# Optimization experiments

Hardware: AMD Instinct MI355X
Metric: run time of the kernel (lower is better)

## Reference

```python
import jax, jax.numpy as jnp
import numpy as np

P = 2        # patch size (all 3 dims)
NB = 8       # num_bands
N = 16       # d_state
DTR = 8      # dt_rank = d_model // 16
DCONV = 4    # d_conv
SMAX = 2.0   # smax_dt = smax_B = smax_C


def _ln(x, g, b):
    mu = x.mean(-1, keepdims=True)
    v = ((x - mu) ** 2).mean(-1, keepdims=True)
    return (x - mu) / jnp.sqrt(v + 1e-5) * g + b


def _silu(x):
    return x * jax.nn.sigmoid(x)


def _ssm_layer(x, band, m, rho, Win, bin_, convw, convb, Wx, Wdt, bdt, Alog, Dp,
               Wout, bout, edt, eB, eC, wr, wm):
    # x: [B, L, d_model] -> bidirectional conditioned selective scan (BiFCSSM)
    Bsz, L, _ = x.shape
    ED = convw.shape[0]
    xz = x @ Win + bin_
    xp, z = xz[..., :ED], xz[..., ED:]
    # depthwise causal conv1d over L
    xpad = jnp.pad(xp, ((0, 0), (DCONV - 1, 0), (0, 0)))
    xc = sum(xpad[:, k:k + L, :] * convw[:, k] for k in range(DCONV)) + convb
    xc = _silu(xc)
    dbl = xc @ Wx                                    # [B,L,DTR+2N]
    dt = jax.nn.softplus(dbl[..., :DTR] @ Wdt + bdt)  # [B,L,ED]
    # band/radius/mask conditioned modulation of delta, B, C
    s_dt = SMAX * jax.nn.sigmoid(edt[band][None] + wr[0] * rho[None] + wm[0] * m)
    s_B = SMAX * jax.nn.sigmoid(eB[band][None] + wr[1] * rho[None] + wm[1] * m)
    s_C = SMAX * jax.nn.sigmoid(eC[band][None] + wr[2] * rho[None] + wm[2] * m)
    dt = dt * s_dt[..., None]
    Bm = dbl[..., DTR:DTR + N] * s_B[..., None]       # [B,L,N]
    Cm = dbl[..., DTR + N:] * s_C[..., None]          # [B,L,N]
    A = -jnp.exp(Alog)                                # [ED,N]
    dA = jnp.exp(dt[..., None] * A)                   # [B,L,ED,N]
    dBu = (dA - 1.0) / A * Bm[:, :, None, :] * xc[..., None]   # exact ZOH
    dA_s = jnp.moveaxis(dA, 1, 0)
    dBu_s = jnp.moveaxis(dBu, 1, 0)
    C_s = jnp.moveaxis(Cm, 1, 0)
    h0 = jnp.zeros((Bsz, ED, N), x.dtype)

    def step(h, inp):
        a, bu, c = inp
        h = a * h + bu
        return h, jnp.einsum('ben,bn->be', h, c)

    _, yf = jax.lax.scan(step, h0, (dA_s, dBu_s, C_s))
    _, yb = jax.lax.scan(step, h0, (dA_s, dBu_s, C_s), reverse=True)
    y = jnp.moveaxis(yf + yb, 0, 1) + Dp * xc
    y = y * _silu(z)
    return y @ Wout + bout


def _fwd(kspace_ri, mask, pe_w, pe_b, pu_w, pu_b, ln_g, ln_b, fn_g, fn_b,
         cond_band, cond_rad_w, cond_mask_w, l0_Win, l0_bin, l0_convw, l0_convb,
         l0_Wx, l0_Wdt, l0_bdt, l0_Alog, l0_D, l0_Wout, l0_bout, l0_edt, l0_eB,
         l0_eC, l0_wr, l0_wm):
    Bsz, C, nx, ny, nz = kspace_ri.shape
    gx, gy, gz = nx // P, ny // P, nz // P
    L = gx * gy * gz
    # patch embed (Conv3d, kernel==stride) as blocked einsum
    xr = kspace_ri.reshape(Bsz, C, gx, P, gy, P, gz, P)
    x = jnp.einsum('bcxiyjzk,dcijk->bdxyz', xr, pe_w) + pe_b[None, :, None, None, None]
    DM = x.shape[1]
    x = x.reshape(Bsz, DM, L).transpose(0, 2, 1)               # [B,L,D]
    m = mask.reshape(Bsz, 1, gx, P, gy, P, gz, P).mean(axis=(3, 5, 7)).reshape(Bsz, L)
    m = jnp.clip(m, 0.0, 1.0)
    # raster scan ordering: identity permutation, rho_bar, band ids
    rho = jnp.arange(L, dtype=x.dtype) / float(L - 1)
    band = jnp.clip(jnp.floor(rho * NB).astype(jnp.int32), 0, NB - 1)
    # condition tokens
    cond = cond_band[band][None] + rho[None, :, None] * cond_rad_w + m[:, :, None] * cond_mask_w
    h = _ln(x + cond, ln_g, ln_b)
    h = h + _ssm_layer(_ln(h, fn_g, fn_b), band, m, rho, l0_Win, l0_bin, l0_convw,
                       l0_convb, l0_Wx, l0_Wdt, l0_bdt, l0_Alog, l0_D, l0_Wout,
                       l0_bout, l0_edt, l0_eB, l0_eC, l0_wr, l0_wm)
    # patch unembed (ConvTranspose3d, kernel==stride) as blocked einsum
    hg = h.transpose(0, 2, 1).reshape(Bsz, DM, gx, gy, gz)
    out = jnp.einsum('bdxyz,dcijk->bcxiyjzk', hg, pu_w).reshape(Bsz, C, nx, ny, nz)
    out = out + pu_b[None, :, None, None, None]
    return kspace_ri + out


def setup_inputs() -> dict:
    key = jax.random.key(0)
    ks = jax.random.split(key, 24)
    ED, DM, CIN = 256, 128, 16

    def nrm(k, shape, s):
        return jax.random.normal(k, shape, jnp.float32) * s

    return {
        'kspace_ri': jax.random.normal(ks[0], (1, CIN, 64, 64, 16), jnp.float32),
        'mask': jax.random.uniform(ks[1], (1, 1, 64, 64, 16), jnp.float32),
        'pe_w': nrm(ks[2], (DM, CIN, P, P, P), 0.09),
        'pe_b': nrm(ks[3], (DM,), 0.02),
        'pu_w': nrm(ks[4], (DM, CIN, P, P, P), 0.05),
        'pu_b': jnp.zeros((CIN,), jnp.float32),
        'ln_g': jnp.ones((DM,), jnp.float32),
        'ln_b': jnp.zeros((DM,), jnp.float32),
        'fn_g': jnp.ones((DM,), jnp.float32),
        'fn_b': jnp.zeros((DM,), jnp.float32),
        'cond_band': nrm(ks[5], (NB, DM), 0.02),
        'cond_rad_w': nrm(ks[6], (DM,), 0.02),
        'cond_mask_w': nrm(ks[7], (DM,), 0.02),
        'l0_Win': nrm(ks[8], (DM, 2 * ED), 0.05),
        'l0_bin': jnp.zeros((2 * ED,), jnp.float32),
        'l0_convw': nrm(ks[9], (ED, DCONV), 0.2),
        'l0_convb': jnp.zeros((ED,), jnp.float32),
        'l0_Wx': nrm(ks[10], (ED, DTR + 2 * N), 0.05),
        'l0_Wdt': nrm(ks[11], (DTR, ED), 0.1),
        'l0_bdt': jnp.full((ED,), -3.0, jnp.float32),
        'l0_Alog': jnp.log(jnp.tile(jnp.arange(1, N + 1, dtype=jnp.float32), (ED, 1))),
        'l0_D': jnp.ones((ED,), jnp.float32),
        'l0_Wout': nrm(ks[12], (ED, DM), 0.05),
        'l0_bout': jnp.zeros((DM,), jnp.float32),
        'l0_edt': nrm(ks[13], (NB,), 0.1),
        'l0_eB': nrm(ks[14], (NB,), 0.1),
        'l0_eC': nrm(ks[15], (NB,), 0.1),
        'l0_wr': nrm(ks[16], (3,), 0.1),
        'l0_wm': nrm(ks[17], (3,), 0.1),
    }


def reference(kspace_ri, mask, pe_w, pe_b, pu_w, pu_b, ln_g, ln_b, fn_g, fn_b,
              cond_band, cond_rad_w, cond_mask_w, l0_Win, l0_bin, l0_convw,
              l0_convb, l0_Wx, l0_Wdt, l0_bdt, l0_Alog, l0_D, l0_Wout, l0_bout,
              l0_edt, l0_eB, l0_eC, l0_wr, l0_wm):
    return _fwd(kspace_ri, mask, pe_w, pe_b, pu_w, pu_b, ln_g, ln_b, fn_g, fn_b,
                cond_band, cond_rad_w, cond_mask_w, l0_Win, l0_bin, l0_convw,
                l0_convb, l0_Wx, l0_Wdt, l0_bdt, l0_Alog, l0_D, l0_Wout, l0_bout,
                l0_edt, l0_eB, l0_eC, l0_wr, l0_wm)
```

## Files before the change

### kernel.cpp

```cpp
#include <hip/hip_runtime.h>
#include <hip/hip_bf16.h>

#define L_TOK 8192
#define NCh 256
#define CLh 32
#define LOG2E 1.44269504088896f

typedef short bf16x8 __attribute__((ext_vector_type(8)));
typedef float f32x4 __attribute__((ext_vector_type(4)));

static __device__ __forceinline__ float nexp2(float x) {
#if __has_builtin(__builtin_amdgcn_exp2f)
    return __builtin_amdgcn_exp2f(x);
#else
    return exp2f(x);
#endif
}
static __device__ __forceinline__ float sigm(float x) {
    return 1.f / (1.f + nexp2(-x * LOG2E));
}
static __device__ __forceinline__ ushort f2bf(float x) {
    union { float f; uint u; } v; v.f = x;
    uint r = v.u + 0x7fffu + ((v.u >> 16) & 1u);
    return (ushort)(r >> 16);
}
static __device__ __forceinline__ float bf2f(ushort h) {
    union { float f; uint u; } v; v.u = ((uint)h) << 16;
    return v.f;
}
static __device__ __forceinline__ void f2hl(float x, ushort* hi, ushort* lo) {
    ushort h = f2bf(x);
    *hi = h;
    *lo = f2bf(x - bf2f(h));
}

#define W_PE   0
#define W_WIN  16384
#define W_WOUT 81920
#define W_PU   114688
#define W_PROJ 131072
#define W_TOT  212992

__global__ __launch_bounds__(256) void prep_k(const float* __restrict__ pe_w, const float* __restrict__ Win,
                                              const float* __restrict__ Wx, const float* __restrict__ Wdt,
                                              const float* __restrict__ Wout, const float* __restrict__ pu_w,
                                              const float* __restrict__ mask,
                                              ushort* __restrict__ wH, ushort* __restrict__ wL,
                                              float* __restrict__ mbuf) {
    int b = blockIdx.x;
    if (b >= 832) {
        int l = (b - 832) * 256 + threadIdx.x;
        int xg = l >> 8, yg = (l >> 3) & 31, zg = l & 7;
        float s = 0.f;
        for (int i2 = 0; i2 < 2; ++i2)
            for (int j2 = 0; j2 < 2; ++j2)
                for (int k2 = 0; k2 < 2; ++k2)
                    s += mask[(2 * xg + i2) * 1024 + (2 * yg + j2) * 16 + 2 * zg + k2];
        s *= 0.125f;
        mbuf[l] = fminf(fmaxf(s, 0.f), 1.f);
        return;
    }
    int i = b * 256 + threadIdx.x;
    float v;
    if (i < 16384) {
        v = pe_w[i];
    } else if (i < 81920) {
        int j = i - 16384; int n = j >> 7, k = j & 127;
        v = Win[k * 512 + n];
    } else if (i < 114688) {
        int j = i - 81920; int n = j >> 8, k = j & 255;
        v = Wout[k * 128 + n];
    } else if (i < 131072) {
        int j = i - 114688; int n = j >> 7, k = j & 127;
        v = pu_w[k * 128 + n];
    } else {
        int j = i - 131072; int n = j >> 8, k = j & 255;
        if (n < 256) {
            float s = 0.f;
#pragma unroll
            for (int r = 0; r < 8; ++r) s += Wx[k * 40 + r] * Wdt[r * 256 + n];
            v = s;
        } else if (n < 288) {
            v = Wx[k * 40 + 8 + (n - 256)];
        } else {
            v = 0.f;
        }
    }
    ushort h, lo; f2hl(v, &h, &lo);
    wH[i] = h; wL[i] = lo;
}

__global__ __launch_bounds__(256) void embed_ln_k(const float* __restrict__ ks,
                                                  const ushort* __restrict__ wH, const ushort* __restrict__ wL,
                                                  const float* __restrict__ pe_b, const float* __restrict__ cond_band,
                                                  const float* __restrict__ cond_rad, const float* __restrict__ cond_mask,
                                                  const float* __restrict__ mbuf,
                                                  const float* __restrict__ ln_g, const float* __restrict__ ln_b,
                                                  const float* __restrict__ fn_g, const float* __restrict__ fn_b,
                                                  float* __restrict__ h_,
                                                  ushort* __restrict__ hnH, ushort* __restrict__ hnL) {
    __shared__ __align__(16) char smem[50176];
    ushort (*AsH)[72] = (ushort(*)[72])(smem);
    ushort (*AsL)[72] = (ushort(*)[72])(smem + 2304);
    ushort (*BsH)[72] = (ushort(*)[72])(smem + 4608);
    ushort (*BsL)[72] = (ushort(*)[72])(smem + 23040);
    float*  ksb       = (float*)(smem + 41472);
    float  (*Cs)[132] = (float(*)[132])(smem);

    const int tid = threadIdx.x;
    const int lane = tid & 63, wn = tid >> 6;
    const int ln = lane & 15, q = lane >> 4;
    const int mb = blockIdx.x * 16;
    const int xg = mb >> 8, yg0 = (mb >> 3) & 31;

    for (int v = tid; v < 512; v += 256) {
        int seg = v >> 2, zq = v & 3;
        int cc = seg >> 3, i2 = (seg >> 2) & 1, yy = seg & 3;
        float4 t4 = *(const float4*)&ks[cc * 65536 + (2 * xg + i2) * 1024 + (2 * yg0 + yy) * 16 + zq * 4];
        int la = seg * 17 + zq * 4;
        ksb[la] = t4.x; ksb[la + 1] = t4.y; ksb[la + 2] = t4.z; ksb[la + 3] = t4.w;
    }

    f32x4 acc[2];
    acc[0] = (f32x4){0.f, 0.f, 0.f, 0.f};
    acc[1] = (f32x4){0.f, 0.f, 0.f, 0.f};

    for (int kc = 0; kc < 128; kc += 64) {
        __syncthreads();
        for (int u = tid; u < 1024; u += 256) {
            int r = u >> 6, kk = u & 63;
            int k = kc + kk;
            int cc = k >> 3, ijk = k & 7;
            int i2 = (ijk >> 2) & 1, j2 = (ijk >> 1) & 1, k2 = ijk & 1;
            int seg = (cc * 2 + i2) * 4 + (r >> 3) * 2 + j2;
            float v = ksb[seg * 17 + (r & 7) * 2 + k2];
            ushort hh, ll; f2hl(v, &hh, &ll);
            AsH[r][kk] = hh; AsL[r][kk] = ll;
        }
        for (int u = tid; u < 1024; u += 256) {
            int n = u >> 3, g = u & 7;
            *(uint4*)&BsH[n][g * 8] = *(const uint4*)&wH[W_PE + n * 128 + kc + g * 8];
            *(uint4*)&BsL[n][g * 8] = *(const uint4*)&wL[W_PE + n * 128 + kc + g * 8];
        }
        __syncthreads();
#pragma unroll
        for (int ks_ = 0; ks_ < 64; ks_ += 32) {
            const int kk = ks_ + q * 8;
            bf16x8 ah = *(const bf16x8*)&AsH[ln][kk];
            bf16x8 al = *(const bf16x8*)&AsL[ln][kk];
#pragma unroll
            for (int cb = 0; cb < 2; ++cb) {
                bf16x8 bh = *(const bf16x8*)&BsH[wn * 32 + cb * 16 + ln][kk];
                bf16x8 bl = *(const bf16x8*)&BsL[wn * 32 + cb * 16 + ln][kk];
                acc[cb] = __builtin_amdgcn_mfma_f32_16x16x32_bf16(ah, bh, acc[cb], 0, 0, 0);
                acc[cb] = __builtin_amdgcn_mfma_f32_16x16x32_bf16(ah, bl, acc[cb], 0, 0, 0);
                acc[cb] = __builtin_amdgcn_mfma_f32_16x16x32_bf16(al, bh, acc[cb], 0, 0, 0);
            }
        }
    }
    __syncthreads();
#pragma unroll
    for (int cb = 0; cb < 2; ++cb) {
#pragma unroll
        for (int r = 0; r < 4; ++r) {
            int row = q * 4 + r;
            int col = wn * 32 + cb * 16 + ln;
            int l = mb + row;
            float rho = (float)l * (1.0f / 8191.0f);
            int band = min(7, (int)(rho * 8.0f));
            Cs[row][col] = acc[cb][r] + pe_b[col] + cond_band[band * 128 + col]
                           + rho * cond_rad[col] + mbuf[l] * cond_mask[col];
        }
    }
    __syncthreads();
    {
        int row = tid >> 4, j = tid & 15;
        int l = mb + row;
        float v8[8];
        float s = 0.f, s2 = 0.f;
#pragma unroll
        for (int i = 0; i < 8; ++i) {
            float v = Cs[row][j * 8 + i];
            v8[i] = v; s += v; s2 += v * v;
        }
#pragma unroll
        for (int o = 1; o < 16; o <<= 1) { s += __shfl_xor(s, o, 16); s2 += __shfl_xor(s2, o, 16); }
        float mu = s * (1.f / 128.f);
        float var = s2 * (1.f / 128.f) - mu * mu;
        float rstd = rsqrtf(fmaxf(var, 0.f) + 1e-5f);
        float hv[8];
        s = 0.f; s2 = 0.f;
#pragma unroll
        for (int i = 0; i < 8; ++i) {
            int col = j * 8 + i;
            float h = (v8[i] - mu) * rstd * ln_g[col] + ln_b[col];
            hv[i] = h; s += h; s2 += h * h;
        }
#pragma unroll
        for (int i = 0; i < 8; i += 4)
            *(float4*)&h_[(size_t)l * 128 + j * 8 + i] = make_float4(hv[i], hv[i + 1], hv[i + 2], hv[i + 3]);
#pragma unroll
        for (int o = 1; o < 16; o <<= 1) { s += __shfl_xor(s, o, 16); s2 += __shfl_xor(s2, o, 16); }
        mu = s * (1.f / 128.f);
        var = s2 * (1.f / 128.f) - mu * mu;
        rstd = rsqrtf(fmaxf(var, 0.f) + 1e-5f);
        union { ushort u[8]; uint4 v4; } oh, ol;
#pragma unroll
        for (int i = 0; i < 8; ++i) {
            int col = j * 8 + i;
            float o2 = (hv[i] - mu) * rstd * fn_g[col] + fn_b[col];
            ushort hh, ll; f2hl(o2, &hh, &ll);
            oh.u[i] = hh; ol.u[i] = ll;
        }
        *(uint4*)&hnH[(size_t)l * 128 + j * 8] = oh.v4;
        *(uint4*)&hnL[(size_t)l * 128 + j * 8] = ol.v4;
    }
}

__global__ __launch_bounds__(256) void win_k(const ushort* __restrict__ Ah, const ushort* __restrict__ Al,
                                             const ushort* __restrict__ wH, const ushort* __restrict__ wL,
                                             const float* __restrict__ bin_,
                                             float* __restrict__ xp, float* __restrict__ sz) {
    __shared__ ushort AsH[64][72], AsL[64][72];
    __shared__ ushort BsH[64][72], BsL[64][72];
    const int tid = threadIdx.x;
    const int lane = tid & 63, wave = tid >> 6;
    const int wm = wave & 1, wn = wave >> 1;
    const int ln = lane & 15, q = lane >> 4;
    const int mb = blockIdx.x * 64, nb = blockIdx.y * 64;

    f32x4 acc[2][2];
#pragma unroll
    for (int rb = 0; rb < 2; ++rb)
#pragma unroll
        for (int cb = 0; cb < 2; ++cb) acc[rb][cb] = (f32x4){0.f, 0.f, 0.f, 0.f};

    for (int kc = 0; kc < 128; kc += 64) {
        __syncthreads();
        for (int u = tid; u < 512; u += 256) {
            int r = u >> 3, g = u & 7;
            size_t go = (size_t)(mb + r) * 128 + kc + g * 8;
            *(uint4*)&AsH[r][g * 8] = *(const uint4*)&Ah[go];
            *(uint4*)&AsL[r][g * 8] = *(const uint4*)&Al[go];
        }
        for (int u = tid; u < 512; u += 256) {
            int n = u >> 3, g = u & 7;
            size_t go = (size_t)(W_WIN) + (size_t)(nb + n) * 128 + kc + g * 8;
            *(uint4*)&BsH[n][g * 8] = *(const uint4*)&wH[go];
            *(uint4*)&BsL[n][g * 8] = *(const uint4*)&wL[go];
        }
        __syncthreads();
#pragma unroll
        for (int ks_ = 0; ks_ < 64; ks_ += 32) {
            const int kk = ks_ + q * 8;
            bf16x8 ah[2], al[2], bh[2], bl[2];
#pragma unroll
            for (int rb = 0; rb < 2; ++rb) {
                ah[rb] = *(const bf16x8*)&AsH[wm * 32 + rb * 16 + ln][kk];
                al[rb] = *(const bf16x8*)&AsL[wm * 32 + rb * 16 + ln][kk];
            }
#pragma unroll
            for (int cb = 0; cb < 2; ++cb) {
                bh[cb] = *(const bf16x8*)&BsH[wn * 32 + cb * 16 + ln][kk];
                bl[cb] = *(const bf16x8*)&BsL[wn * 32 + cb * 16 + ln][kk];
            }
#pragma unroll
            for (int rb = 0; rb < 2; ++rb)
#pragma unroll
                for (int cb = 0; cb < 2; ++cb) {
                    acc[rb][cb] = __builtin_amdgcn_mfma_f32_16x16x32_bf16(ah[rb], bh[cb], acc[rb][cb], 0, 0, 0);
                    acc[rb][cb] = __builtin_amdgcn_mfma_f32_16x16x32_bf16(ah[rb], bl[cb], acc[rb][cb], 0, 0, 0);
                    acc[rb][cb] = __builtin_amdgcn_mfma_f32_16x16x32_bf16(al[rb], bh[cb], acc[rb][cb], 0, 0, 0);
                }
        }
    }
#pragma unroll
    for (int rb = 0; rb < 2; ++rb)
#pragma unroll
        for (int cb = 0; cb < 2; ++cb)
#pragma unroll
            for (int r = 0; r < 4; ++r) {
                int l = mb + wm * 32 + rb * 16 + q * 4 + r;
                int col = nb + wn * 32 + cb * 16 + ln;
                float v = acc[rb][cb][r] + bin_[col];
                if (col < 256) {
                    xp[(size_t)l * 256 + col] = v;
                } else {
                    sz[(size_t)l * 256 + (col - 256)] = v * sigm(v);
                }
            }
}

__global__ __launch_bounds__(512) void proj_k(const float* __restrict__ xp,
                                              const float* __restrict__ convw, const float* __restrict__ convb,
                                              const ushort* __restrict__ wH, const ushort* __restrict__ wL,
                                              const float* __restrict__ bdt, const float* __restrict__ mbuf,
                                              const float* __restrict__ edt, const float* __restrict__ eB,
                                              const float* __restrict__ eC, const float* __restrict__ wr,
                                              const float* __restrict__ wm,
                                              float* __restrict__ xc, float* __restrict__ dt,
                                              float* __restrict__ Bm, float* __restrict__ Cm) {
    __shared__ __align__(16) char smem[52224];
    ushort (*AsH)[264] = (ushort(*)[264])(smem);
    ushort (*AsL)[264] = (ushort(*)[264])(smem + 16896);
    ushort (*BsH)[72]  = (ushort(*)[72])(smem + 33792);
    ushort (*BsL)[72]  = (ushort(*)[72])(smem + 43008);
    const int tid = threadIdx.x;
    const int mb = blockIdx.x * 32;

    {
        const int cg = tid & 63;
        const int rg = tid >> 6;
        const int c0 = cg * 4;
        float4 cb4 = *(const float4*)&convb[c0];
        float4 cw0 = *(const float4*)&convw[(c0 + 0) * 4];
        float4 cw1 = *(const float4*)&convw[(c0 + 1) * 4];
        float4 cw2 = *(const float4*)&convw[(c0 + 2) * 4];
        float4 cw3 = *(const float4*)&convw[(c0 + 3) * 4];
        const int lbase = mb + rg * 4;
        float4 zero = make_float4(0.f, 0.f, 0.f, 0.f);
        float4 x0 = (lbase - 3 >= 0) ? *(const float4*)&xp[(size_t)(lbase - 3) * 256 + c0] : zero;
        float4 x1 = (lbase - 2 >= 0) ? *(const float4*)&xp[(size_t)(lbase - 2) * 256 + c0] : zero;
        float4 x2 = (lbase - 1 >= 0) ? *(const float4*)&xp[(size_t)(lbase - 1) * 256 + c0] : zero;
#pragma unroll
        for (int rr = 0; rr < 4; ++rr) {
            int l = lbase + rr;
            float4 x3 = *(const float4*)&xp[(size_t)l * 256 + c0];
            float o0 = cb4.x + x0.x * cw0.x + x1.x * cw0.y + x2.x * cw0.z + x3.x * cw0.w;
            float o1 = cb4.y + x0.y * cw1.x + x1.y * cw1.y + x2.y * cw1.z + x3.y * cw1.w;
            float o2 = cb4.z + x0.z * cw2.x + x1.z * cw2.y + x2.z * cw2.z + x3.z * cw2.w;
            float o3 = cb4.w + x0.w * cw3.x + x1.w * cw3.y + x2.w * cw3.z + x3.w * cw3.w;
            o0 *= sigm(o0); o1 *= sigm(o1); o2 *= sigm(o2); o3 *= sigm(o3);
            *(float4*)&xc[(size_t)l * 256 + c0] = make_float4(o0, o1, o2, o3);
            union { ushort u[4]; uint2 v2; } hh, ll;
            f2hl(o0, &hh.u[0], &ll.u[0]); f2hl(o1, &hh.u[1], &ll.u[1]);
            f2hl(o2, &hh.u[2], &ll.u[2]); f2hl(o3, &hh.u[3], &ll.u[3]);
            int row = l - mb;
            *(uint2*)&AsH[row][c0] = hh.v2;
            *(uint2*)&AsL[row][c0] = ll.v2;
            x0 = x1; x1 = x2; x2 = x3;
        }
    }
    __syncthreads();

    const int lane = tid & 63, wave = tid >> 6;
    const int wm2 = wave & 1, wn4 = wave >> 1;
    const int ln = lane & 15, q = lane >> 4;
    for (int it = 0; it < 5; ++it) {
        int nb = it * 64;
        f32x4 acc = (f32x4){0.f, 0.f, 0.f, 0.f};
        for (int kc = 0; kc < 256; kc += 64) {
            __syncthreads();
            {
                int u = tid;
                int n = u >> 3, g = u & 7;
                size_t go = (size_t)(W_PROJ) + (size_t)(nb + n) * 256 + kc + g * 8;
                *(uint4*)&BsH[n][g * 8] = *(const uint4*)&wH[go];
                *(uint4*)&BsL[n][g * 8] = *(const uint4*)&wL[go];
            }
            __syncthreads();
#pragma unroll
            for (int ks_ = 0; ks_ < 64; ks_ += 32) {
                const int kka = kc + ks_ + q * 8;
                const int kkb = ks_ + q * 8;
                bf16x8 ah = *(const bf16x8*)&AsH[wm2 * 16 + ln][kka];
                bf16x8 al = *(const bf16x8*)&AsL[wm2 * 16 + ln][kka];
                bf16x8 bh = *(const bf16x8*)&BsH[wn4 * 16 + ln][kkb];
                bf16x8 bl = *(const bf16x8*)&BsL[wn4 * 16 + ln][kkb];
                acc = __builtin_amdgcn_mfma_f32_16x16x32_bf16(ah, bh, acc, 0, 0, 0);
                acc = __builtin_amdgcn_mfma_f32_16x16x32_bf16(ah, bl, acc, 0, 0, 0);
                acc = __builtin_amdgcn_mfma_f32_16x16x32_bf16(al, bh, acc, 0, 0, 0);
            }
        }
#pragma unroll
        for (int r = 0; r < 4; ++r) {
            int l = mb + wm2 * 16 + q * 4 + r;
            int col = nb + wn4 * 16 + ln;
            float v = acc[r];
            float rho = (float)l * (1.0f / 8191.0f);
            int band = min(7, (int)(rho * 8.0f));
            float mv = mbuf[l];
            if (col < 256) {
                float sc0 = 2.0f * sigm(edt[band] + wr[0] * rho + wm[0] * mv);
                float v2 = v + bdt[col];
                float sp = (v2 > 20.f) ? v2 : log1pf(expf(v2));
                dt[(size_t)l * 256 + col] = sp * sc0;
            } else if (col < 272) {
                float sc1 = 2.0f * sigm(eB[band] + wr[1] * rho + wm[1] * mv);
                Bm[(size_t)l * 16 + (col - 256)] = v * sc1;
            } else if (col < 288) {
                float sc2 = 2.0f * sigm(eC[band] + wr[2] * rho + wm[2] * mv);
                Cm[(size_t)l * 16 + (col - 272)] = v * sc2;
            }
        }
    }
}

__global__ __launch_bounds__(256) void scan0_k(const float* __restrict__ dt, const float* __restrict__ xc,
                                               const float* __restrict__ Bm, const float* __restrict__ Alog,
                                               float* __restrict__ Hb, float* __restrict__ sdtb) {
    const int c = blockIdx.x, dir = blockIdx.y, e = threadIdx.x;
    __shared__ float bms[CLh][16];
    for (int idx = e; idx < CLh * 16; idx += 256)
        bms[idx >> 4][idx & 15] = Bm[c * (CLh * 16) + idx];
    float A2[16], iv[16], h[16];
#pragma unroll
    for (int n = 0; n < 16; ++n) {
        float ea = nexp2(Alog[e * 16 + n] * LOG2E);
        A2[n] = -ea * LOG2E;
        iv[n] = -1.0f / ea;
        h[n] = 0.f;
    }
    const int base = c * CLh;
    float cu[8], cx[8], nu[8], nx[8];
#pragma unroll
    for (int j = 0; j < 8; ++j) {
        int p = dir ? (CLh - 1 - j) : j;
        cu[j] = dt[(size_t)(base + p) * 256 + e];
        cx[j] = xc[(size_t)(base + p) * 256 + e];
    }
    __syncthreads();
    float sdt = 0.f;
#pragma unroll
    for (int g = 0; g < CLh / 8; ++g) {
        if (g + 1 < CLh / 8) {
#pragma unroll
            for (int j = 0; j < 8; ++j) {
                int s = (g + 1) * 8 + j;
                int p = dir ? (CLh - 1 - s) : s;
                nu[j] = dt[(size_t)(base + p) * 256 + e];
                nx[j] = xc[(size_t)(base + p) * 256 + e];
            }
        }
#pragma unroll
        for (int j = 0; j < 8; ++j) {
            int s = g * 8 + j;
            int p = dir ? (CLh - 1 - s) : s;
            float u = cu[j], xv = cx[j];
            union { float4 v[4]; float f[16]; } bb;
            const float4* bp = (const float4*)&bms[p][0];
            bb.v[0] = bp[0]; bb.v[1] = bp[1]; bb.v[2] = bp[2]; bb.v[3] = bp[3];
#pragma unroll
            for (int n = 0; n < 16; ++n) {
                float a = nexp2(A2[n] * u);
                float w = xv * bb.f[n] * iv[n];
                h[n] = a * (h[n] + w) - w;
            }
            sdt += u;
        }
#pragma unroll
        for (int j = 0; j < 8; ++j) { cu[j] = nu[j]; cx[j] = nx[j]; }
    }
    const size_t hofs = (size_t)(dir * NCh + c) * 4096 + e * 16;
#pragma unroll
    for (int j = 0; j < 4; ++j)
        *(float4*)&Hb[hofs + 4 * j] = make_float4(h[4 * j], h[4 * j + 1], h[4 * j + 2], h[4 * j + 3]);
    if (dir == 0) sdtb[c * 256 + e] = sdt;
}

__global__ __launch_bounds__(64) void combine_k(const float* __restrict__ Hb, float* __restrict__ Hpre,
                                                const float* __restrict__ sdtb, const float* __restrict__ Alog) {
    int id = blockIdx.x * 64 + threadIdx.x;
    int dir = id >> 12, en = id & 4095, e = en >> 4;
    float A2 = -nexp2(Alog[en] * LOG2E) * LOG2E;
    float hi = 0.f;
    for (int g = 0; g < NCh / 8; ++g) {
        float Pv[8], qv[8];
#pragma unroll
        for (int j = 0; j < 8; ++j) {
            int c = dir ? (NCh - 1 - (g * 8 + j)) : (g * 8 + j);
            Pv[j] = sdtb[c * 256 + e];
            qv[j] = Hb[(size_t)(dir * NCh + c) * 4096 + en];
        }
#pragma unroll
        for (int j = 0; j < 8; ++j) {
            int c = dir ? (NCh - 1 - (g * 8 + j)) : (g * 8 + j);
            float P = nexp2(A2 * Pv[j]);
            Hpre[(size_t)(dir * NCh + c) * 4096 + en] = hi;
            hi = P * hi + qv[j];
        }
    }
}

template <int DIR>
static __device__ __forceinline__ void scan_dir(const float* __restrict__ dt, const float* __restrict__ xc,
                                                int base, int e,
                                                const float (*bms)[16], const float (*cms)[16],
                                                const float* A2, const float* iv,
                                                float* h, float* yreg) {
    float cu[8], cx[8], nu[8], nx[8];
#pragma unroll
    for (int j = 0; j < 8; ++j) {
        const int p = DIR ? (CLh - 1 - j) : j;
        cu[j] = dt[(size_t)(base + p) * 256 + e];
        cx[j] = xc[(size_t)(base + p) * 256 + e];
    }
#pragma unroll
    for (int g = 0; g < CLh / 8; ++g) {
        if (g + 1 < CLh / 8) {
#pragma unroll
            for (int j = 0; j < 8; ++j) {
                const int s = (g + 1) * 8 + j;
                const int p = DIR ? (CLh - 1 - s) : s;
                nu[j] = dt[(size_t)(base + p) * 256 + e];
                nx[j] = xc[(size_t)(base + p) * 256 + e];
            }
        }
#pragma unroll
        for (int j = 0; j < 8; ++j) {
            const int s = g * 8 + j;
            const int p = DIR ? (CLh - 1 - s) : s;
            float u = cu[j], xv = cx[j];
            union { float4 v[4]; float f[16]; } bb, cc;
            const float4* bp = (const float4*)&bms[p][0];
            bb.v[0] = bp[0]; bb.v[1] = bp[1]; bb.v[2] = bp[2]; bb.v[3] = bp[3];
            const float4* cp = (const float4*)&cms[p][0];
            cc.v[0] = cp[0]; cc.v[1] = cp[1]; cc.v[2] = cp[2]; cc.v[3] = cp[3];
            float y = 0.f;
#pragma unroll
            for (int n = 0; n < 16; ++n) {
                float a = nexp2(A2[n] * u);
                float w = xv * bb.f[n] * iv[n];
                h[n] = a * (h[n] + w) - w;
                y += h[n] * cc.f[n];
            }
            yreg[p] = y;
        }
#pragma unroll
        for (int j = 0; j < 8; ++j) { cu[j] = nu[j]; cx[j] = nx[j]; }
    }
}

__global__ __launch_bounds__(512) void scan1g_k(const float* __restrict__ dt, const float* __restrict__ xc,
                                                const float* __restrict__ Bm, const float* __restrict__ Cm,
                                                const float* __restrict__ Alog, const float* __restrict__ Hpre,
                                                const float* __restrict__ sz, const float* __restrict__ Dp,
                                                ushort* __restrict__ AHo, ushort* __restrict__ ALo) {
    const int c = blockIdx.x;
    const int tid = threadIdx.x;
    const int dir = tid >> 8;
    const int e = tid & 255;
    __shared__ float bms[CLh][16];
    __shared__ float cms[CLh][16];
    __shared__ float ysum[CLh][256];
    for (int idx = tid; idx < CLh * 16; idx += 512) {
        bms[idx >> 4][idx & 15] = Bm[c * (CLh * 16) + idx];
        cms[idx >> 4][idx & 15] = Cm[c * (CLh * 16) + idx];
    }
    float A2[16], iv[16], h[16];
#pragma unroll
    for (int n = 0; n < 16; ++n) {
        float ea = nexp2(Alog[e * 16 + n] * LOG2E);
        A2[n] = -ea * LOG2E;
        iv[n] = -1.0f / ea;
    }
    const size_t hofs = (size_t)(dir * NCh + c) * 4096 + e * 16;
#pragma unroll
    for (int j = 0; j < 4; ++j) {
        float4 hv = *(const float4*)&Hpre[hofs + 4 * j];
        h[4 * j] = hv.x; h[4 * j + 1] = hv.y; h[4 * j + 2] = hv.z; h[4 * j + 3] = hv.w;
    }
    const int base = c * CLh;
    float yreg[CLh];
    __syncthreads();
    if (dir == 0) {
        scan_dir<0>(dt, xc, base, e, bms, cms, A2, iv, h, yreg);
    } else {
        scan_dir<1>(dt, xc, base, e, bms, cms, A2, iv, h, yreg);
    }
    __syncthreads();
    if (dir == 0) {
#pragma unroll
        for (int l = 0; l < CLh; ++l) ysum[l][e] = yreg[l];
    }
    __syncthreads();
    if (dir == 1) {
        float dpv = Dp[e];
#pragma unroll
        for (int l = 0; l < CLh; ++l) {
            size_t gl = (size_t)(base + l) * 256 + e;
            float a = (ysum[l][e] + yreg[l] + dpv * xc[gl]) * sz[gl];
            ushort hh, ll; f2hl(a, &hh, &ll);
            AHo[gl] = hh; ALo[gl] = ll;
        }
    }
}

__global__ __launch_bounds__(256) void wout_k(const ushort* __restrict__ AH, const ushort* __restrict__ AL,
                                              const ushort* __restrict__ wH, const ushort* __restrict__ wL,
                                              const float* __restrict__ bout, const float* __restrict__ h_,
                                              ushort* __restrict__ hfH, ushort* __restrict__ hfL) {
    __shared__ ushort AsH[32][72], AsL[32][72];
    __shared__ ushort BsH[64][72], BsL[64][72];
    const int tid = threadIdx.x;
    const int lane = tid & 63, wave = tid >> 6;
    const int wm = wave & 1, wn = wave >> 1;
    const int ln = lane & 15, q = lane >> 4;
    const int mb = blockIdx.x * 32, nb = blockIdx.y * 64;

    f32x4 acc[2];
    acc[0] = (f32x4){0.f, 0.f, 0.f, 0.f};
    acc[1] = (f32x4){0.f, 0.f, 0.f, 0.f};

    for (int kc = 0; kc < 256; kc += 64) {
        __syncthreads();
        for (int u = tid; u < 256; u += 256) {
            int r = u >> 3, g = u & 7;
            size_t go = (size_t)(mb + r) * 256 + kc + g * 8;
            *(uint4*)&AsH[r][g * 8] = *(const uint4*)&AH[go];
            *(uint4*)&AsL[r][g * 8] = *(const uint4*)&AL[go];
        }
        for (int u = tid; u < 512; u += 256) {
            int n = u >> 3, g = u & 7;
            size_t go = (size_t)(W_WOUT) + (size_t)(nb + n) * 256 + kc + g * 8;
            *(uint4*)&BsH[n][g * 8] = *(const uint4*)&wH[go];
            *(uint4*)&BsL[n][g * 8] = *(const uint4*)&wL[go];
        }
        __syncthreads();
#pragma unroll
        for (int ks_ = 0; ks_ < 64; ks_ += 32) {
            const int kk = ks_ + q * 8;
            bf16x8 ah = *(const bf16x8*)&AsH[wm * 16 + ln][kk];
            bf16x8 al = *(const bf16x8*)&AsL[wm * 16 + ln][kk];
#pragma unroll
            for (int cb = 0; cb < 2; ++cb) {
                bf16x8 bh = *(const bf16x8*)&BsH[wn * 32 + cb * 16 + ln][kk];
                bf16x8 bl = *(const bf16x8*)&BsL[wn * 32 + cb * 16 + ln][kk];
                acc[cb] = __builtin_amdgcn_mfma_f32_16x16x32_bf16(ah, bh, acc[cb], 0, 0, 0);
                acc[cb] = __builtin_amdgcn_mfma_f32_16x16x32_bf16(ah, bl, acc[cb], 0, 0, 0);
                acc[cb] = __builtin_amdgcn_mfma_f32_16x16x32_bf16(al, bh, acc[cb], 0, 0, 0);
            }
        }
    }
#pragma unroll
    for (int cb = 0; cb < 2; ++cb)
#pragma unroll
        for (int r = 0; r < 4; ++r) {
            int l = mb + wm * 16 + q * 4 + r;
            int col = nb + wn * 32 + cb * 16 + ln;
            float v = acc[cb][r] + bout[col] + h_[(size_t)l * 128 + col];
            ushort hh, ll; f2hl(v, &hh, &ll);
            hfH[(size_t)l * 128 + col] = hh;
            hfL[(size_t)l * 128 + col] = ll;
        }
}

__global__ __launch_bounds__(256) void unembed_k(const ushort* __restrict__ Ah, const ushort* __restrict__ Al,
                                                 const ushort* __restrict__ wH, const ushort* __restrict__ wL,
                                                 const float* __restrict__ pu_b, const float* __restrict__ ks,
                                                 float* __restrict__ out) {
    __shared__ ushort AsH[32][72], AsL[32][72];
    __shared__ ushort BsH[64][72], BsL[64][72];
    const int tid = threadIdx.x;
    const int lane = tid & 63, wave = tid >> 6;
    const int wm = wave & 1, wn = wave >> 1;
    const int ln = lane & 15, q = lane >> 4;
    const int mb = blockIdx.x * 32, nb = blockIdx.y * 64;

    f32x4 acc[2];
    acc[0] = (f32x4){0.f, 0.f, 0.f, 0.f};
    acc[1] = (f32x4){0.f, 0.f, 0.f, 0.f};

    for (int kc = 0; kc < 128; kc += 64) {
        __syncthreads();
        for (int u = tid; u < 256; u += 256) {
            int r = u >> 3, g = u & 7;
            size_t go = (size_t)(mb + r) * 128 + kc + g * 8;
            *(uint4*)&AsH[r][g * 8] = *(const uint4*)&Ah[go];
            *(uint4*)&AsL[r][g * 8] = *(const uint4*)&Al[go];
        }
        for (int u = tid; u < 512; u += 256) {
            int n = u >> 3, g = u & 7;
            size_t go = (size_t)(W_PU) + (size_t)(nb + n) * 128 + kc + g * 8;
            *(uint4*)&BsH[n][g * 8] = *(const uint4*)&wH[go];
            *(uint4*)&BsL[n][g * 8] = *(const uint4*)&wL[go];
        }
        __syncthreads();
#pragma unroll
        for (int ks_ = 0; ks_ < 64; ks_ += 32) {
            const int kk = ks_ + q * 8;
            bf16x8 ah = *(const bf16x8*)&AsH[wm * 16 + ln][kk];
            bf16x8 al = *(const bf16x8*)&AsL[wm * 16 + ln][kk];
#pragma unroll
            for (int cb = 0; cb < 2; ++cb) {
                bf16x8 bh = *(const bf16x8*)&BsH[wn * 32 + cb * 16 + ln][kk];
                bf16x8 bl = *(const bf16x8*)&BsL[wn * 32 + cb * 16 + ln][kk];
                acc[cb] = __builtin_amdgcn_mfma_f32_16x16x32_bf16(ah, bh, acc[cb], 0, 0, 0);
                acc[cb] = __builtin_amdgcn_mfma_f32_16x16x32_bf16(ah, bl, acc[cb], 0, 0, 0);
                acc[cb] = __builtin_amdgcn_mfma_f32_16x16x32_bf16(al, bh, acc[cb], 0, 0, 0);
            }
        }
    }
#pragma unroll
    for (int cb = 0; cb < 2; ++cb)
#pragma unroll
        for (int r = 0; r < 4; ++r) {
            int l = mb + wm * 16 + q * 4 + r;
            int col = nb + wn * 32 + cb * 16 + ln;
            int xg = l >> 8, yg = (l >> 3) & 31, zg = l & 7;
            int c = col >> 3, ijk = col & 7;
            int i2 = (ijk >> 2) & 1, j2 = (ijk >> 1) & 1, k2 = ijk & 1;
            size_t idx = (size_t)((c * 64 + 2 * xg + i2) * 64 + (2 * yg + j2)) * 16 + 2 * zg + k2;
            out[idx] = acc[cb][r] + pu_b[c] + ks[idx];
        }
}

extern "C" void kernel_launch(void* const* d_in, const int* in_sizes, int n_in,
                              void* d_out, int out_size, void* d_ws, size_t ws_size,
                              hipStream_t stream) {
    const float* ks    = (const float*)d_in[0];
    const float* mask  = (const float*)d_in[1];
    const float* pe_w  = (const float*)d_in[2];
    const float* pe_b  = (const float*)d_in[3];
    const float* pu_w  = (const float*)d_in[4];
    const float* pu_b  = (const float*)d_in[5];
    const float* ln_g  = (const float*)d_in[6];
    const float* ln_b  = (const float*)d_in[7];
    const float* fn_g  = (const float*)d_in[8];
    const float* fn_b  = (const float*)d_in[9];
    const float* cond_band = (const float*)d_in[10];
    const float* cond_rad  = (const float*)d_in[11];
    const float* cond_mask = (const float*)d_in[12];
    const float* Win   = (const float*)d_in[13];
    const float* bin_  = (const float*)d_in[14];
    const float* convw = (const float*)d_in[15];
    const float* convb = (const float*)d_in[16];
    const float* Wx    = (const float*)d_in[17];
    const float* Wdt   = (const float*)d_in[18];
    const float* bdt   = (const float*)d_in[19];
    const float* Alog  = (const float*)d_in[20];
    const float* Dp    = (const float*)d_in[21];
    const float* Wout  = (const float*)d_in[22];
    const float* bout  = (const float*)d_in[23];
    const float* edt   = (const float*)d_in[24];
    const float* eB    = (const float*)d_in[25];
    const float* eC    = (const float*)d_in[26];
    const float* wr    = (const float*)d_in[27];
    const float* wm    = (const float*)d_in[28];
    float* out = (float*)d_out;

    char* base = (char*)d_ws;
    size_t o = 0;
    auto alloc = [&](size_t bytes) { char* p = base + o; o += (bytes + 255) & ~(size_t)255; return p; };
    float*  mbuf = (float*)alloc(32768);
    ushort* wH   = (ushort*)alloc(W_TOT * 2);
    ushort* wL   = (ushort*)alloc(W_TOT * 2);
    float*  h_   = (float*)alloc(4194304);
    ushort* hnH  = (ushort*)alloc(2097152);
    ushort* hnL  = (ushort*)alloc(2097152);
    float*  xp   = (float*)alloc(8388608);
    float*  sz   = (float*)alloc(8388608);
    float*  xc   = (float*)alloc(8388608);
    float*  dt   = (float*)alloc(8388608);
    float*  Bm   = (float*)alloc(524288);
    float*  Cm   = (float*)alloc(524288);
    float*  Hb   = (float*)alloc(8388608);
    float*  Hpre = (float*)alloc(8388608);
    float*  sdtb = (float*)alloc(262144);
    ushort* AHo  = (ushort*)alloc(4194304);
    ushort* ALo  = (ushort*)alloc(4194304);
    ushort* hfH  = (ushort*)alloc(2097152);
    ushort* hfL  = (ushort*)alloc(2097152);

    prep_k<<<864, 256, 0, stream>>>(pe_w, Win, Wx, Wdt, Wout, pu_w, mask, wH, wL, mbuf);
    embed_ln_k<<<512, 256, 0, stream>>>(ks, wH, wL, pe_b, cond_band, cond_rad, cond_mask, mbuf,
                                        ln_g, ln_b, fn_g, fn_b, h_, hnH, hnL);
    win_k<<<dim3(128, 8), 256, 0, stream>>>(hnH, hnL, wH, wL, bin_, xp, sz);
    proj_k<<<256, 512, 0, stream>>>(xp, convw, convb, wH, wL, bdt, mbuf, edt, eB, eC, wr, wm,
                                    xc, dt, Bm, Cm);
    scan0_k<<<dim3(NCh, 2), 256, 0, stream>>>(dt, xc, Bm, Alog, Hb, sdtb);
    combine_k<<<128, 64, 0, stream>>>(Hb, Hpre, sdtb, Alog);
    scan1g_k<<<NCh, 512, 0, stream>>>(dt, xc, Bm, Cm, Alog, Hpre, sz, Dp, AHo, ALo);
    wout_k<<<dim3(256, 2), 256, 0, stream>>>(AHo, ALo, wH, wL, bout, h_, hfH, hfL);
    unembed_k<<<dim3(256, 2), 256, 0, stream>>>(hfH, hfL, wH, wL, pu_b, ks, out);
}
```

Measured before the change: 237.4 us.

## Fuse Wout and unembed GEMMs into one kernel with LDS-resident intermediate

Merges the output projection and the unembedding GEMM into a single kernel. Each block holds a 32-row A tile across the full K in LDS, computes all 128 output columns, and keeps the residual-added hidden state as a bf16 hi/lo pair in shared memory instead of writing it to global and reading it back. The combine kernel's chunk loop is also widened from 8 to 16 loads in flight. The cost is half as many blocks (256 instead of 512) and about 52 KB of LDS per block, which lowers parallelism and occupancy.

New measurement: 243.5 us. 2.6% more time.

```diff
diff --git a/kernel.cpp b/kernel.cpp
--- a/kernel.cpp
+++ b/kernel.cpp
@@ -464,17 +464,17 @@
     int dir = id >> 12, en = id & 4095, e = en >> 4;
     float A2 = -nexp2(Alog[en] * LOG2E) * LOG2E;
     float hi = 0.f;
-    for (int g = 0; g < NCh / 8; ++g) {
-        float Pv[8], qv[8];
-#pragma unroll
-        for (int j = 0; j < 8; ++j) {
-            int c = dir ? (NCh - 1 - (g * 8 + j)) : (g * 8 + j);
+    for (int g = 0; g < NCh / 16; ++g) {
+        float Pv[16], qv[16];
+#pragma unroll
+        for (int j = 0; j < 16; ++j) {
+            int c = dir ? (NCh - 1 - (g * 16 + j)) : (g * 16 + j);
             Pv[j] = sdtb[c * 256 + e];
             qv[j] = Hb[(size_t)(dir * NCh + c) * 4096 + en];
         }
 #pragma unroll
-        for (int j = 0; j < 8; ++j) {
-            int c = dir ? (NCh - 1 - (g * 8 + j)) : (g * 8 + j);
+        for (int j = 0; j < 16; ++j) {
+            int c = dir ? (NCh - 1 - (g * 16 + j)) : (g * 16 + j);
             float P = nexp2(A2 * Pv[j]);
             Hpre[(size_t)(dir * NCh + c) * 4096 + en] = hi;
             hi = P * hi + qv[j];
@@ -586,123 +586,130 @@
     }
 }
 
-__global__ __launch_bounds__(256) void wout_k(const ushort* __restrict__ AH, const ushort* __restrict__ AL,
-                                              const ushort* __restrict__ wH, const ushort* __restrict__ wL,
-                                              const float* __restrict__ bout, const float* __restrict__ h_,
-                                              ushort* __restrict__ hfH, ushort* __restrict__ hfL) {
-    __shared__ ushort AsH[32][72], AsL[32][72];
-    __shared__ ushort BsH[64][72], BsL[64][72];
+__global__ __launch_bounds__(256) void wu_k(const ushort* __restrict__ AH, const ushort* __restrict__ AL,
+                                            const ushort* __restrict__ wH, const ushort* __restrict__ wL,
+                                            const float* __restrict__ bout, const float* __restrict__ h_,
+                                            const float* __restrict__ pu_b, const float* __restrict__ ks,
+                                            float* __restrict__ out) {
+    __shared__ __align__(16) char smem[52224];
+    ushort (*AsH)[264] = (ushort(*)[264])(smem);
+    ushort (*AsL)[264] = (ushort(*)[264])(smem + 16896);
+    ushort (*BsH)[72]  = (ushort(*)[72])(smem + 33792);
+    ushort (*BsL)[72]  = (ushort(*)[72])(smem + 43008);
+    ushort (*hfH)[136] = (ushort(*)[136])(smem + 33792);
+    ushort (*hfL)[136] = (ushort(*)[136])(smem + 42496);
+
     const int tid = threadIdx.x;
     const int lane = tid & 63, wave = tid >> 6;
     const int wm = wave & 1, wn = wave >> 1;
     const int ln = lane & 15, q = lane >> 4;
-    const int mb = blockIdx.x * 32, nb = blockIdx.y * 64;
-
-    f32x4 acc[2];
-    acc[0] = (f32x4){0.f, 0.f, 0.f, 0.f};
-    acc[1] = (f32x4){0.f, 0.f, 0.f, 0.f};
-
-    for (int kc = 0; kc < 256; kc += 64) {
-        __syncthreads();
-        for (int u = tid; u < 256; u += 256) {
-            int r = u >> 3, g = u & 7;
-            size_t go = (size_t)(mb + r) * 256 + kc + g * 8;
-            *(uint4*)&AsH[r][g * 8] = *(const uint4*)&AH[go];
-            *(uint4*)&AsL[r][g * 8] = *(const uint4*)&AL[go];
-        }
-        for (int u = tid; u < 512; u += 256) {
-            int n = u >> 3, g = u & 7;
-            size_t go = (size_t)(W_WOUT) + (size_t)(nb + n) * 256 + kc + g * 8;
-            *(uint4*)&BsH[n][g * 8] = *(const uint4*)&wH[go];
-            *(uint4*)&BsL[n][g * 8] = *(const uint4*)&wL[go];
-        }
-        __syncthreads();
-#pragma unroll
-        for (int ks_ = 0; ks_ < 64; ks_ += 32) {
-            const int kk = ks_ + q * 8;
-            bf16x8 ah = *(const bf16x8*)&AsH[wm * 16 + ln][kk];
-            bf16x8 al = *(const bf16x8*)&AsL[wm * 16 + ln][kk];
-#pragma unroll
-            for (int cb = 0; cb < 2; ++cb) {
-                bf16x8 bh = *(const bf16x8*)&BsH[wn * 32 + cb * 16 + ln][kk];
-                bf16x8 bl = *(const bf16x8*)&BsL[wn * 32 + cb * 16 + ln][kk];
-                acc[cb] = __builtin_amdgcn_mfma_f32_16x16x32_bf16(ah, bh, acc[cb], 0, 0, 0);
-                acc[cb] = __builtin_amdgcn_mfma_f32_16x16x32_bf16(ah, bl, acc[cb], 0, 0, 0);
-                acc[cb] = __builtin_amdgcn_mfma_f32_16x16x32_bf16(al, bh, acc[cb], 0, 0, 0);
-            }
-        }
-    }
-#pragma unroll
-    for (int cb = 0; cb < 2; ++cb)
-#pragma unroll
-        for (int r = 0; r < 4; ++r) {
-            int l = mb + wm * 16 + q * 4 + r;
-            int col = nb + wn * 32 + cb * 16 + ln;
-            float v = acc[cb][r] + bout[col] + h_[(size_t)l * 128 + col];
-            ushort hh, ll; f2hl(v, &hh, &ll);
-            hfH[(size_t)l * 128 + col] = hh;
-            hfL[(size_t)l * 128 + col] = ll;
-        }
-}
-
-__global__ __launch_bounds__(256) void unembed_k(const ushort* __restrict__ Ah, const ushort* __restrict__ Al,
-                                                 const ushort* __restrict__ wH, const ushort* __restrict__ wL,
-                                                 const float* __restrict__ pu_b, const float* __restrict__ ks,
-                                                 float* __restrict__ out) {
-    __shared__ ushort AsH[32][72], AsL[32][72];
-    __shared__ ushort BsH[64][72], BsL[64][72];
-    const int tid = threadIdx.x;
-    const int lane = tid & 63, wave = tid >> 6;
-    const int wm = wave & 1, wn = wave >> 1;
-    const int ln = lane & 15, q = lane >> 4;
-    const int mb = blockIdx.x * 32, nb = blockIdx.y * 64;
-
-    f32x4 acc[2];
-    acc[0] = (f32x4){0.f, 0.f, 0.f, 0.f};
-    acc[1] = (f32x4){0.f, 0.f, 0.f, 0.f};
-
-    for (int kc = 0; kc < 128; kc += 64) {
-        __syncthreads();
-        for (int u = tid; u < 256; u += 256) {
-            int r = u >> 3, g = u & 7;
-            size_t go = (size_t)(mb + r) * 128 + kc + g * 8;
-            *(uint4*)&AsH[r][g * 8] = *(const uint4*)&Ah[go];
-            *(uint4*)&AsL[r][g * 8] = *(const uint4*)&Al[go];
-        }
-        for (int u = tid; u < 512; u += 256) {
-            int n = u >> 3, g = u & 7;
-            size_t go = (size_t)(W_PU) + (size_t)(nb + n) * 128 + kc + g * 8;
-            *(uint4*)&BsH[n][g * 8] = *(const uint4*)&wH[go];
-            *(uint4*)&BsL[n][g * 8] = *(const uint4*)&wL[go];
-        }
-        __syncthreads();
-#pragma unroll
-        for (int ks_ = 0; ks_ < 64; ks_ += 32) {
-            const int kk = ks_ + q * 8;
-            bf16x8 ah = *(const bf16x8*)&AsH[wm * 16 + ln][kk];
-            bf16x8 al = *(const bf16x8*)&AsL[wm * 16 + ln][kk];
-#pragma unroll
-            for (int cb = 0; cb < 2; ++cb) {
-                bf16x8 bh = *(const bf16x8*)&BsH[wn * 32 + cb * 16 + ln][kk];
-                bf16x8 bl = *(const bf16x8*)&BsL[wn * 32 + cb * 16 + ln][kk];
-                acc[cb] = __builtin_amdgcn_mfma_f32_16x16x32_bf16(ah, bh, acc[cb], 0, 0, 0);
-                acc[cb] = __builtin_amdgcn_mfma_f32_16x16x32_bf16(ah, bl, acc[cb], 0, 0, 0);
-                acc[cb] = __builtin_amdgcn_mfma_f32_16x16x32_bf16(al, bh, acc[cb], 0, 0, 0);
-            }
-        }
-    }
-#pragma unroll
-    for (int cb = 0; cb < 2; ++cb)
-#pragma unroll
-        for (int r = 0; r < 4; ++r) {
-            int l = mb + wm * 16 + q * 4 + r;
-            int col = nb + wn * 32 + cb * 16 + ln;
-            int xg = l >> 8, yg = (l >> 3) & 31, zg = l & 7;
-            int c = col >> 3, ijk = col & 7;
-            int i2 = (ijk >> 2) & 1, j2 = (ijk >> 1) & 1, k2 = ijk & 1;
-            size_t idx = (size_t)((c * 64 + 2 * xg + i2) * 64 + (2 * yg + j2)) * 16 + 2 * zg + k2;
-            out[idx] = acc[cb][r] + pu_b[c] + ks[idx];
-        }
+    const int mb = blockIdx.x * 32;
+
+    for (int u = tid; u < 1024; u += 256) {
+        int r = u >> 5, g = u & 31;
+        size_t go = (size_t)(mb + r) * 256 + g * 8;
+        *(uint4*)&AsH[r][g * 8] = *(const uint4*)&AH[go];
+        *(uint4*)&AsL[r][g * 8] = *(const uint4*)&AL[go];
+    }
+
+    f32x4 acc[2][2];
+#pragma unroll
+    for (int hf_ = 0; hf_ < 2; ++hf_)
+#pragma unroll
+        for (int cb = 0; cb < 2; ++cb) acc[hf_][cb] = (f32x4){0.f, 0.f, 0.f, 0.f};
+
+#pragma unroll
+    for (int half = 0; half < 2; ++half) {
+        int nb = half * 64;
+        for (int kc = 0; kc < 256; kc += 64) {
+            __syncthreads();
+            for (int u = tid; u < 512; u += 256) {
+                int n = u >> 3, g = u & 7;
+                size_t go = (size_t)(W_WOUT) + (size_t)(nb + n) * 256 + kc + g * 8;
+                *(uint4*)&BsH[n][g * 8] = *(const uint4*)&wH[go];
+                *(uint4*)&BsL[n][g * 8] = *(const uint4*)&wL[go];
+            }
+            __syncthreads();
+#pragma unroll
+            for (int ks_ = 0; ks_ < 64; ks_ += 32) {
+                const int kka = kc + ks_ + q * 8;
+                const int kkb = ks_ + q * 8;
+                bf16x8 ah = *(const bf16x8*)&AsH[wm * 16 + ln][kka];
+                bf16x8 al = *(const bf16x8*)&AsL[wm * 16 + ln][kka];
+#pragma unroll
+                for (int cb = 0; cb < 2; ++cb) {
+                    bf16x8 bh = *(const bf16x8*)&BsH[wn * 32 + cb * 16 + ln][kkb];
+                    bf16x8 bl = *(const bf16x8*)&BsL[wn * 32 + cb * 16 + ln][kkb];
+                    acc[half][cb] = __builtin_amdgcn_mfma_f32_16x16x32_bf16(ah, bh, acc[half][cb], 0, 0, 0);
+                    acc[half][cb] = __builtin_amdgcn_mfma_f32_16x16x32_bf16(ah, bl, acc[half][cb], 0, 0, 0);
+                    acc[half][cb] = __builtin_amdgcn_mfma_f32_16x16x32_bf16(al, bh, acc[half][cb], 0, 0, 0);
+                }
+            }
+        }
+    }
+    __syncthreads();
+#pragma unroll
+    for (int half = 0; half < 2; ++half)
+#pragma unroll
+        for (int cb = 0; cb < 2; ++cb)
+#pragma unroll
+            for (int r = 0; r < 4; ++r) {
+                int row = wm * 16 + q * 4 + r;
+                int col = half * 64 + wn * 32 + cb * 16 + ln;
+                int l = mb + row;
+                float v = acc[half][cb][r] + bout[col] + h_[(size_t)l * 128 + col];
+                ushort hh, ll; f2hl(v, &hh, &ll);
+                hfH[row][col] = hh;
+                hfL[row][col] = ll;
+            }
+    __syncthreads();
+
+    ushort (*UbH)[72] = (ushort(*)[72])(smem);
+    ushort (*UbL)[72] = (ushort(*)[72])(smem + 9216);
+#pragma unroll
+    for (int half = 0; half < 2; ++half) {
+        int nb = half * 64;
+        f32x4 ua[2];
+        ua[0] = (f32x4){0.f, 0.f, 0.f, 0.f};
+        ua[1] = (f32x4){0.f, 0.f, 0.f, 0.f};
+        for (int kc = 0; kc < 128; kc += 64) {
+            __syncthreads();
+            for (int u = tid; u < 512; u += 256) {
+                int n = u >> 3, g = u & 7;
+                size_t go = (size_t)(W_PU) + (size_t)(nb + n) * 128 + kc + g * 8;
+                *(uint4*)&UbH[n][g * 8] = *(const uint4*)&wH[go];
+                *(uint4*)&UbL[n][g * 8] = *(const uint4*)&wL[go];
+            }
+            __syncthreads();
+#pragma unroll
+            for (int ks_ = 0; ks_ < 64; ks_ += 32) {
+                const int kka = kc + ks_ + q * 8;
+                const int kkb = ks_ + q * 8;
+                bf16x8 ah = *(const bf16x8*)&hfH[wm * 16 + ln][kka];
+                bf16x8 al = *(const bf16x8*)&hfL[wm * 16 + ln][kka];
+#pragma unroll
+                for (int cb = 0; cb < 2; ++cb) {
+                    bf16x8 bh = *(const bf16x8*)&UbH[wn * 32 + cb * 16 + ln][kkb];
+                    bf16x8 bl = *(const bf16x8*)&UbL[wn * 32 + cb * 16 + ln][kkb];
+                    ua[cb] = __builtin_amdgcn_mfma_f32_16x16x32_bf16(ah, bh, ua[cb], 0, 0, 0);
+                    ua[cb] = __builtin_amdgcn_mfma_f32_16x16x32_bf16(ah, bl, ua[cb], 0, 0, 0);
+                    ua[cb] = __builtin_amdgcn_mfma_f32_16x16x32_bf16(al, bh, ua[cb], 0, 0, 0);
+                }
+            }
+        }
+#pragma unroll
+        for (int cb = 0; cb < 2; ++cb)
+#pragma unroll
+            for (int r = 0; r < 4; ++r) {
+                int l = mb + wm * 16 + q * 4 + r;
+                int col = nb + wn * 32 + cb * 16 + ln;
+                int xg = l >> 8, yg = (l >> 3) & 31, zg = l & 7;
+                int c = col >> 3, ijk = col & 7;
+                int i2 = (ijk >> 2) & 1, j2 = (ijk >> 1) & 1, k2 = ijk & 1;
+                size_t idx = (size_t)((c * 64 + 2 * xg + i2) * 64 + (2 * yg + j2)) * 16 + 2 * zg + k2;
+                out[idx] = ua[cb][r] + pu_b[c] + ks[idx];
+            }
+    }
 }
 
 extern "C" void kernel_launch(void* const* d_in, const int* in_sizes, int n_in,
@@ -759,8 +766,6 @@
     float*  sdtb = (float*)alloc(262144);
     ushort* AHo  = (ushort*)alloc(4194304);
     ushort* ALo  = (ushort*)alloc(4194304);
-    ushort* hfH  = (ushort*)alloc(2097152);
-    ushort* hfL  = (ushort*)alloc(2097152);
 
     prep_k<<<864, 256, 0, stream>>>(pe_w, Win, Wx, Wdt, Wout, pu_w, mask, wH, wL, mbuf);
     embed_ln_k<<<512, 256, 0, stream>>>(ks, wH, wL, pe_b, cond_band, cond_rad, cond_mask, mbuf,
@@ -771,6 +776,5 @@
     scan0_k<<<dim3(NCh, 2), 256, 0, stream>>>(dt, xc, Bm, Alog, Hb, sdtb);
     combine_k<<<128, 64, 0, stream>>>(Hb, Hpre, sdtb, Alog);
     scan1g_k<<<NCh, 512, 0, stream>>>(dt, xc, Bm, Cm, Alog, Hpre, sz, Dp, AHo, ALo);
-    wout_k<<<dim3(256, 2), 256, 0, stream>>>(AHo, ALo, wH, wL, bout, h_, hfH, hfL);
-    unembed_k<<<dim3(256, 2), 256, 0, stream>>>(hfH, hfL, wH, wL, pu_b, ks, out);
-}
+    wu_k<<<256, 256, 0, stream>>>(AHo, ALo, wH, wL, bout, h_, pu_b, ks, out);
+}
```
